# Performance work log

Measured on AMD Instinct MI355X. Metric: run time of the kernel, lower is better.

The kernel has to match this reference:

```python
import jax, jax.numpy as jnp
import numpy as np

B = 65536
EPS = 1e-5


def _cnot(psi, c, t):
    # psi: [B,2,2,2,2]; qubit q lives on axis q+1. CNOT flips target where control=1.
    c_ax, t_ax = c + 1, t + 1
    p0 = jax.lax.index_in_dim(psi, 0, c_ax, keepdims=True)
    p1 = jax.lax.index_in_dim(psi, 1, c_ax, keepdims=True)
    p1 = jnp.flip(p1, axis=t_ax)
    return jnp.concatenate([p0, p1], axis=c_ax)


def setup_inputs() -> dict:
    key = jax.random.key(0)
    x = jax.random.normal(key, (B, 1, 28, 28), dtype=jnp.float32)
    gamma = jnp.ones((4,), jnp.float32)   # BatchNorm1d(4) weight
    beta = jnp.zeros((4,), jnp.float32)   # BatchNorm1d(4) bias
    return {"x": x, "gamma": gamma, "beta": beta}


def reference(x, gamma, beta):
    bsz = x.shape[0]
    # avg_pool2d(x, 6): kernel=stride=6, no padding -> uses only the top-left 24x24
    pooled = x[:, :, :24, :24].reshape(bsz, 1, 4, 6, 4, 6).mean(axis=(3, 5))
    pooled = pooled.reshape(bsz, 16)
    theta = pooled[:, ::4]  # x[:, i*4] for i=0..3 -> [B,4] RY angles
    half = 0.5 * theta
    q = jnp.stack([jnp.cos(half), jnp.sin(half)], axis=-1)  # [B,4,2], RY|0> amplitudes (real)
    psi = jnp.einsum('bi,bj,bk,bl->bijkl', q[:, 0], q[:, 1], q[:, 2], q[:, 3])
    for c, t in ((0, 1), (1, 2), (2, 3), (3, 0)):
        psi = _cnot(psi, c, t)
    probs = psi * psi  # amplitudes are real
    signs = jnp.array([1.0, -1.0], jnp.float32)
    # <Z_i> = sum_s probs[s] * (-1)^{s_i}
    zs = [jnp.tensordot(probs, signs, axes=[[i + 1], [0]]).sum(axis=(1, 2, 3))
          for i in range(4)]
    out = jnp.stack(zs, axis=1)  # [B,4]
    # BatchNorm1d(4), training mode (biased batch variance)
    mean = out.mean(axis=0)
    var = out.var(axis=0)
    return gamma * (out - mean) / jnp.sqrt(var + EPS) + beta
```

## Files before the change

### kernel.cpp

```cpp
#include <hip/hip_runtime.h>

#define EPS 1e-5f


__global__ __launch_bounds__(256) void qnat_k1(const float* __restrict__ x,
                                               float* __restrict__ z_out,
                                               float* __restrict__ partials,
                                               int bsz) {
    const int t    = threadIdx.x;
    const int lane = t & 63;
    const int w    = t >> 6;
    const int imgBase = blockIdx.x * 16;

    float s1[4] = {0.f, 0.f, 0.f, 0.f};
    float s2[4] = {0.f, 0.f, 0.f, 0.f};

    #pragma unroll
    for (int iter = 0; iter < 4; ++iter) {
        const int img = imgBase + iter * 4 + w;
        float a0 = 0.f, a1 = 0.f, a2 = 0.f, a3 = 0.f;
        if (img < bsz) {
            const float* ip = x + (size_t)img * 784;
            #pragma unroll
            for (int r = 0; r < 3; ++r) {
                const int j = r * 64 + lane;
                const float4 v = *reinterpret_cast<const float4*>(ip + 4 * j);
                const int m = j % 7;
                const int p = j / 42;
                float contrib = 0.f;
                if (m == 0)      contrib = (v.x + v.y) + (v.z + v.w);
                else if (m == 1) contrib = v.x + v.y;
                a0 += (p == 0) ? contrib : 0.f;
                a1 += (p == 1) ? contrib : 0.f;
                a2 += (p == 2) ? contrib : 0.f;
                a3 += (p == 3) ? contrib : 0.f;
            }
        }
        #pragma unroll
        for (int off = 1; off < 64; off <<= 1) {
            a0 += __shfl_xor(a0, off, 64);
            a1 += __shfl_xor(a1, off, 64);
            a2 += __shfl_xor(a2, off, 64);
            a3 += __shfl_xor(a3, off, 64);
        }
        const float k = 1.0f / 36.0f;
        const float c0 = cosf(a0 * k), c1 = cosf(a1 * k);
        const float c2 = cosf(a2 * k), c3 = cosf(a3 * k);
        const float z1 = c0 * c1;
        const float z2 = z1 * c2;
        const float z3 = z2 * c3;
        const float z0 = c1 * c2 * c3;
        if (img < bsz) {
            if (lane == 0) {
                float4 zz; zz.x = z0; zz.y = z1; zz.z = z2; zz.w = z3;
                *reinterpret_cast<float4*>(z_out + (size_t)img * 4) = zz;
            }
            s1[0] += z0; s1[1] += z1; s1[2] += z2; s1[3] += z3;
            s2[0] += z0 * z0; s2[1] += z1 * z1; s2[2] += z2 * z2; s2[3] += z3 * z3;
        }
    }

    __shared__ float ps[4][8];
    if (lane == 0) {
        #pragma unroll
        for (int k = 0; k < 4; ++k) { ps[w][k] = s1[k]; ps[w][4 + k] = s2[k]; }
    }
    __syncthreads();
    if (t < 8) {
        partials[blockIdx.x * 8 + t] =
            (ps[0][t] + ps[1][t]) + (ps[2][t] + ps[3][t]);
    }
}

__global__ __launch_bounds__(1024) void qnat_stats(const float* __restrict__ partials,
                                                   const float* __restrict__ gamma,
                                                   float* __restrict__ stats,
                                                   int NB, int bsz) {
    const int t = threadIdx.x;
    float acc[8] = {0.f,0.f,0.f,0.f,0.f,0.f,0.f,0.f};
    for (int r = t; r < NB; r += 1024) {
        const float4 a = *reinterpret_cast<const float4*>(partials + r * 8);
        const float4 b = *reinterpret_cast<const float4*>(partials + r * 8 + 4);
        acc[0] += a.x; acc[1] += a.y; acc[2] += a.z; acc[3] += a.w;
        acc[4] += b.x; acc[5] += b.y; acc[6] += b.z; acc[7] += b.w;
    }
    #pragma unroll
    for (int off = 1; off < 64; off <<= 1)
        #pragma unroll
        for (int k = 0; k < 8; ++k) acc[k] += __shfl_xor(acc[k], off, 64);

    __shared__ float ls[16][8];
    const int wv = t >> 6, lane = t & 63;
    if (lane == 0)
        #pragma unroll
        for (int k = 0; k < 8; ++k) ls[wv][k] = acc[k];
    __syncthreads();
    if (t < 8) {
        float tot = 0.f;
        #pragma unroll
        for (int v = 0; v < 16; ++v) tot += ls[v][t];
        ls[0][t] = tot;
    }
    __syncthreads();
    if (t < 4) {
        const double invB = 1.0 / (double)bsz;
        const double m = (double)ls[0][t] * invB;
        const double var = (double)ls[0][4 + t] * invB - m * m;
        stats[t]     = (float)m;
        stats[4 + t] = gamma[t] * rsqrtf((float)var + EPS);
    }
}

__global__ __launch_bounds__(256) void qnat_k2(const float* __restrict__ z,
                                               const float* __restrict__ stats,
                                               const float* __restrict__ beta,
                                               float* __restrict__ out,
                                               int bsz) {
    const int t = blockIdx.x * blockDim.x + threadIdx.x;
    if (t < bsz) {
        const float4 zv = reinterpret_cast<const float4*>(z)[t];
        float4 o;
        o.x = (zv.x - stats[0]) * stats[4] + beta[0];
        o.y = (zv.y - stats[1]) * stats[5] + beta[1];
        o.z = (zv.z - stats[2]) * stats[6] + beta[2];
        o.w = (zv.w - stats[3]) * stats[7] + beta[3];
        reinterpret_cast<float4*>(out)[t] = o;
    }
}

extern "C" void kernel_launch(void* const* d_in, const int* in_sizes, int n_in,
                              void* d_out, int out_size, void* d_ws, size_t ws_size,
                              hipStream_t stream) {
    const float* x     = (const float*)d_in[0];
    const float* gamma = (const float*)d_in[1];
    const float* beta  = (const float*)d_in[2];
    float* out = (float*)d_out;

    const int bsz = in_sizes[0] / 784;
    const int NB  = (bsz + 15) / 16;

    float* stats    = (float*)d_ws;
    float* z        = (float*)((char*)d_ws + 4096);
    float* partials = (float*)((char*)d_ws + 4096 + (size_t)bsz * 16);

    qnat_k1   <<<NB, 256, 0, stream>>>(x, z, partials, bsz);
    qnat_stats<<<1, 1024, 0, stream>>>(partials, gamma, stats, NB, bsz);
    qnat_k2   <<<(bsz + 255) / 256, 256, 0, stream>>>(z, stats, beta, out, bsz);
}
```

Before: 45.74 us.

## Fuse pooling, batch stats and normalization into one cooperative grid-synced kernel

Replaces three launches (per-image kernel, single-block stats reduction, normalize pass) with one cooperative kernel of 1024 blocks. Each block keeps its z values in shared memory, writes per-block partial sums, waits at a grid-wide sync, then reduces all partials and normalizes its own images, so the z round trip through global memory and two launch gaps go away. It also skips the unused float4 loads in the last row group and swaps cosf for the faster, less accurate __cosf. The grid sync adds its own cost, and the hardcoded ipb cap of 64 means batches larger than 65536 would be silently truncated.

```diff
diff --git a/kernel.cpp b/kernel.cpp
--- a/kernel.cpp
+++ b/kernel.cpp
@@ -1,39 +1,53 @@
 #include <hip/hip_runtime.h>
+#include <hip/hip_cooperative_groups.h>
+
+namespace cg = cooperative_groups;
 
 #define EPS 1e-5f
+#define NBLK 1024
 
 
-__global__ __launch_bounds__(256) void qnat_k1(const float* __restrict__ x,
-                                               float* __restrict__ z_out,
-                                               float* __restrict__ partials,
-                                               int bsz) {
+__global__ __launch_bounds__(256, 4) void qnat_fused(const float* __restrict__ x,
+                                                     const float* __restrict__ gamma,
+                                                     const float* __restrict__ beta,
+                                                     float* __restrict__ out,
+                                                     float* __restrict__ partials,
+                                                     int bsz, int ipb) {
+    __shared__ float zsh[64][4];
+    __shared__ float ps[4][8];
+    __shared__ float red[4][8];
+    __shared__ float st[8];
+
     const int t    = threadIdx.x;
     const int lane = t & 63;
     const int w    = t >> 6;
-    const int imgBase = blockIdx.x * 16;
+    const int ipw  = ipb >> 2;
+    const int blk0 = blockIdx.x * ipb;
 
-    float s1[4] = {0.f, 0.f, 0.f, 0.f};
-    float s2[4] = {0.f, 0.f, 0.f, 0.f};
+    float s1[4] = {0.f,0.f,0.f,0.f};
+    float s2[4] = {0.f,0.f,0.f,0.f};
 
-    #pragma unroll
-    for (int iter = 0; iter < 4; ++iter) {
-        const int img = imgBase + iter * 4 + w;
+    for (int i = 0; i < ipw; ++i) {
+        const int il  = w * ipw + i;
+        const int img = blk0 + il;
         float a0 = 0.f, a1 = 0.f, a2 = 0.f, a3 = 0.f;
         if (img < bsz) {
             const float* ip = x + (size_t)img * 784;
             #pragma unroll
             for (int r = 0; r < 3; ++r) {
                 const int j = r * 64 + lane;
-                const float4 v = *reinterpret_cast<const float4*>(ip + 4 * j);
-                const int m = j % 7;
-                const int p = j / 42;
-                float contrib = 0.f;
-                if (m == 0)      contrib = (v.x + v.y) + (v.z + v.w);
-                else if (m == 1) contrib = v.x + v.y;
-                a0 += (p == 0) ? contrib : 0.f;
-                a1 += (p == 1) ? contrib : 0.f;
-                a2 += (p == 2) ? contrib : 0.f;
-                a3 += (p == 3) ? contrib : 0.f;
+                if (r < 2 || lane < 40) {
+                    const float4 v = *reinterpret_cast<const float4*>(ip + 4 * j);
+                    const int m = j % 7;
+                    const int p = j / 42;
+                    float contrib = 0.f;
+                    if (m == 0)      contrib = (v.x + v.y) + (v.z + v.w);
+                    else if (m == 1) contrib = v.x + v.y;
+                    a0 += (p == 0) ? contrib : 0.f;
+                    a1 += (p == 1) ? contrib : 0.f;
+                    a2 += (p == 2) ? contrib : 0.f;
+                    a3 += (p == 3) ? contrib : 0.f;
+                }
             }
         }
         #pragma unroll
@@ -44,8 +58,8 @@
             a3 += __shfl_xor(a3, off, 64);
         }
         const float k = 1.0f / 36.0f;
-        const float c0 = cosf(a0 * k), c1 = cosf(a1 * k);
-        const float c2 = cosf(a2 * k), c3 = cosf(a3 * k);
+        const float c0 = __cosf(a0 * k), c1 = __cosf(a1 * k);
+        const float c2 = __cosf(a2 * k), c3 = __cosf(a3 * k);
         const float z1 = c0 * c1;
         const float z2 = z1 * c2;
         const float z3 = z2 * c3;
@@ -53,78 +67,59 @@
         if (img < bsz) {
             if (lane == 0) {
                 float4 zz; zz.x = z0; zz.y = z1; zz.z = z2; zz.w = z3;
-                *reinterpret_cast<float4*>(z_out + (size_t)img * 4) = zz;
+                *reinterpret_cast<float4*>(&zsh[il][0]) = zz;
             }
             s1[0] += z0; s1[1] += z1; s1[2] += z2; s1[3] += z3;
-            s2[0] += z0 * z0; s2[1] += z1 * z1; s2[2] += z2 * z2; s2[3] += z3 * z3;
+            s2[0] += z0*z0; s2[1] += z1*z1; s2[2] += z2*z2; s2[3] += z3*z3;
         }
     }
-
-    __shared__ float ps[4][8];
     if (lane == 0) {
         #pragma unroll
-        for (int k = 0; k < 4; ++k) { ps[w][k] = s1[k]; ps[w][4 + k] = s2[k]; }
+        for (int k = 0; k < 4; ++k) { ps[w][k] = s1[k]; ps[w][4+k] = s2[k]; }
     }
     __syncthreads();
     if (t < 8) {
-        partials[blockIdx.x * 8 + t] =
-            (ps[0][t] + ps[1][t]) + (ps[2][t] + ps[3][t]);
+        partials[blockIdx.x * 8 + t] = (ps[0][t] + ps[1][t]) + (ps[2][t] + ps[3][t]);
     }
-}
 
-__global__ __launch_bounds__(1024) void qnat_stats(const float* __restrict__ partials,
-                                                   const float* __restrict__ gamma,
-                                                   float* __restrict__ stats,
-                                                   int NB, int bsz) {
-    const int t = threadIdx.x;
-    float acc[8] = {0.f,0.f,0.f,0.f,0.f,0.f,0.f,0.f};
-    for (int r = t; r < NB; r += 1024) {
-        const float4 a = *reinterpret_cast<const float4*>(partials + r * 8);
-        const float4 b = *reinterpret_cast<const float4*>(partials + r * 8 + 4);
-        acc[0] += a.x; acc[1] += a.y; acc[2] += a.z; acc[3] += a.w;
-        acc[4] += b.x; acc[5] += b.y; acc[6] += b.z; acc[7] += b.w;
+    cg::this_grid().sync();
+
+    {
+        const int k  = t & 7;
+        const int r0 = t >> 3;
+        float acc = 0.f;
+        #pragma unroll 4
+        for (int i = 0; i < NBLK / 32; ++i) {
+            acc += partials[(r0 + 32 * i) * 8 + k];
+        }
+        acc += __shfl_xor(acc, 8, 64);
+        acc += __shfl_xor(acc, 16, 64);
+        acc += __shfl_xor(acc, 32, 64);
+        if (lane < 8) red[w][lane] = acc;
+        __syncthreads();
+        if (t < 8) st[t] = (red[0][t] + red[1][t]) + (red[2][t] + red[3][t]);
+        __syncthreads();
+        if (t < 4) {
+            const double invB = 1.0 / (double)bsz;
+            const double m   = (double)st[t] * invB;
+            const double var = (double)st[4 + t] * invB - m * m;
+            st[t]     = (float)m;
+            st[4 + t] = gamma[t] * rsqrtf((float)var + EPS);
+        }
+        __syncthreads();
     }
-    #pragma unroll
-    for (int off = 1; off < 64; off <<= 1)
-        #pragma unroll
-        for (int k = 0; k < 8; ++k) acc[k] += __shfl_xor(acc[k], off, 64);
 
-    __shared__ float ls[16][8];
-    const int wv = t >> 6, lane = t & 63;
-    if (lane == 0)
-        #pragma unroll
-        for (int k = 0; k < 8; ++k) ls[wv][k] = acc[k];
-    __syncthreads();
-    if (t < 8) {
-        float tot = 0.f;
-        #pragma unroll
-        for (int v = 0; v < 16; ++v) tot += ls[v][t];
-        ls[0][t] = tot;
-    }
-    __syncthreads();
-    if (t < 4) {
-        const double invB = 1.0 / (double)bsz;
-        const double m = (double)ls[0][t] * invB;
-        const double var = (double)ls[0][4 + t] * invB - m * m;
-        stats[t]     = (float)m;
-        stats[4 + t] = gamma[t] * rsqrtf((float)var + EPS);
-    }
-}
-
-__global__ __launch_bounds__(256) void qnat_k2(const float* __restrict__ z,
-                                               const float* __restrict__ stats,
-                                               const float* __restrict__ beta,
-                                               float* __restrict__ out,
-                                               int bsz) {
-    const int t = blockIdx.x * blockDim.x + threadIdx.x;
-    if (t < bsz) {
-        const float4 zv = reinterpret_cast<const float4*>(z)[t];
-        float4 o;
-        o.x = (zv.x - stats[0]) * stats[4] + beta[0];
-        o.y = (zv.y - stats[1]) * stats[5] + beta[1];
-        o.z = (zv.z - stats[2]) * stats[6] + beta[2];
-        o.w = (zv.w - stats[3]) * stats[7] + beta[3];
-        reinterpret_cast<float4*>(out)[t] = o;
+    if (t < 64 && t < ipb) {
+        const int img = blk0 + t;
+        if (img < bsz) {
+            const float4 zv = *reinterpret_cast<const float4*>(&zsh[t][0]);
+            float4 o;
+            o.x = (zv.x - st[0]) * st[4] + beta[0];
+            o.y = (zv.y - st[1]) * st[5] + beta[1];
+            o.z = (zv.z - st[2]) * st[6] + beta[2];
+            o.w = (zv.w - st[3]) * st[7] + beta[3];
+            *reinterpret_cast<float4*>(out + (size_t)img * 4) = o;
+        }
     }
 }
 
@@ -137,13 +132,14 @@
     float* out = (float*)d_out;
 
     const int bsz = in_sizes[0] / 784;
-    const int NB  = (bsz + 15) / 16;
+    float* partials = (float*)d_ws;
 
-    float* stats    = (float*)d_ws;
-    float* z        = (float*)((char*)d_ws + 4096);
-    float* partials = (float*)((char*)d_ws + 4096 + (size_t)bsz * 16);
+    int ipb = (bsz + NBLK - 1) / NBLK;
+    ipb = (ipb + 3) & ~3;
+    if (ipb > 64) ipb = 64;
 
-    qnat_k1   <<<NB, 256, 0, stream>>>(x, z, partials, bsz);
-    qnat_stats<<<1, 1024, 0, stream>>>(partials, gamma, stats, NB, bsz);
-    qnat_k2   <<<(bsz + 255) / 256, 256, 0, stream>>>(z, stats, beta, out, bsz);
+    void* args[] = { (void*)&x, (void*)&gamma, (void*)&beta, (void*)&out,
+                     (void*)&partials, (void*)&bsz, (void*)&ipb };
+    hipLaunchCooperativeKernel((const void*)qnat_fused, dim3(NBLK), dim3(256),
+                               args, 0, stream);
 }
```

Result: slower. 162.8 us (+255.9%).

## Fuse batch-stat reduction into normalize kernel, skip unused loads, use fast cosine

Applied to the files above, without the earlier changes.

Drops the single-block stats kernel. Every block of the normalize kernel now redundantly reduces all per-block partials (4096 rows) itself, which saves one launch and one serialized step. The image loop also skips float4 loads past the 24 needed rows in its last pass, and cosf is replaced by the faster, lower-precision __cosf. The cost is that each of 256 blocks rereads 128KB of partials, and __cosf may lose accuracy.

```diff
diff --git a/kernel.cpp b/kernel.cpp
--- a/kernel.cpp
+++ b/kernel.cpp
@@ -24,16 +24,18 @@
             #pragma unroll
             for (int r = 0; r < 3; ++r) {
                 const int j = r * 64 + lane;
-                const float4 v = *reinterpret_cast<const float4*>(ip + 4 * j);
-                const int m = j % 7;
-                const int p = j / 42;
-                float contrib = 0.f;
-                if (m == 0)      contrib = (v.x + v.y) + (v.z + v.w);
-                else if (m == 1) contrib = v.x + v.y;
-                a0 += (p == 0) ? contrib : 0.f;
-                a1 += (p == 1) ? contrib : 0.f;
-                a2 += (p == 2) ? contrib : 0.f;
-                a3 += (p == 3) ? contrib : 0.f;
+                if (r < 2 || lane < 40) {
+                    const float4 v = *reinterpret_cast<const float4*>(ip + 4 * j);
+                    const int m = j % 7;
+                    const int p = j / 42;
+                    float contrib = 0.f;
+                    if (m == 0)      contrib = (v.x + v.y) + (v.z + v.w);
+                    else if (m == 1) contrib = v.x + v.y;
+                    a0 += (p == 0) ? contrib : 0.f;
+                    a1 += (p == 1) ? contrib : 0.f;
+                    a2 += (p == 2) ? contrib : 0.f;
+                    a3 += (p == 3) ? contrib : 0.f;
+                }
             }
         }
         #pragma unroll
@@ -44,8 +46,8 @@
             a3 += __shfl_xor(a3, off, 64);
         }
         const float k = 1.0f / 36.0f;
-        const float c0 = cosf(a0 * k), c1 = cosf(a1 * k);
-        const float c2 = cosf(a2 * k), c3 = cosf(a3 * k);
+        const float c0 = __cosf(a0 * k), c1 = __cosf(a1 * k);
+        const float c2 = __cosf(a2 * k), c3 = __cosf(a3 * k);
         const float z1 = c0 * c1;
         const float z2 = z1 * c2;
         const float z3 = z2 * c3;
@@ -67,64 +69,58 @@
     }
     __syncthreads();
     if (t < 8) {
-        partials[blockIdx.x * 8 + t] =
-            (ps[0][t] + ps[1][t]) + (ps[2][t] + ps[3][t]);
+        partials[blockIdx.x * 8 + t] = (ps[0][t] + ps[1][t]) + (ps[2][t] + ps[3][t]);
     }
 }
 
-__global__ __launch_bounds__(1024) void qnat_stats(const float* __restrict__ partials,
-                                                   const float* __restrict__ gamma,
-                                                   float* __restrict__ stats,
-                                                   int NB, int bsz) {
-    const int t = threadIdx.x;
+__global__ __launch_bounds__(256) void qnat_k2(const float* __restrict__ z,
+                                               const float* __restrict__ partials,
+                                               const float* __restrict__ gamma,
+                                               const float* __restrict__ beta,
+                                               float* __restrict__ out,
+                                               int NB, int bsz) {
+    __shared__ float red[4][8];
+    __shared__ float st[8];
+
+    const int t = threadIdx.x, lane = t & 63, w = t >> 6;
+
     float acc[8] = {0.f,0.f,0.f,0.f,0.f,0.f,0.f,0.f};
-    for (int r = t; r < NB; r += 1024) {
+    for (int r = t; r < NB; r += 256) {
         const float4 a = *reinterpret_cast<const float4*>(partials + r * 8);
         const float4 b = *reinterpret_cast<const float4*>(partials + r * 8 + 4);
         acc[0] += a.x; acc[1] += a.y; acc[2] += a.z; acc[3] += a.w;
         acc[4] += b.x; acc[5] += b.y; acc[6] += b.z; acc[7] += b.w;
     }
     #pragma unroll
-    for (int off = 1; off < 64; off <<= 1)
+    for (int off = 1; off < 64; off <<= 1) {
         #pragma unroll
         for (int k = 0; k < 8; ++k) acc[k] += __shfl_xor(acc[k], off, 64);
-
-    __shared__ float ls[16][8];
-    const int wv = t >> 6, lane = t & 63;
-    if (lane == 0)
+    }
+    if (lane == 0) {
         #pragma unroll
-        for (int k = 0; k < 8; ++k) ls[wv][k] = acc[k];
+        for (int k = 0; k < 8; ++k) red[w][k] = acc[k];
+    }
     __syncthreads();
-    if (t < 8) {
-        float tot = 0.f;
-        #pragma unroll
-        for (int v = 0; v < 16; ++v) tot += ls[v][t];
-        ls[0][t] = tot;
-    }
+    if (t < 8) st[t] = (red[0][t] + red[1][t]) + (red[2][t] + red[3][t]);
     __syncthreads();
     if (t < 4) {
         const double invB = 1.0 / (double)bsz;
-        const double m = (double)ls[0][t] * invB;
-        const double var = (double)ls[0][4 + t] * invB - m * m;
-        stats[t]     = (float)m;
-        stats[4 + t] = gamma[t] * rsqrtf((float)var + EPS);
+        const double m   = (double)st[t] * invB;
+        const double var = (double)st[4 + t] * invB - m * m;
+        st[t]     = (float)m;
+        st[4 + t] = gamma[t] * rsqrtf((float)var + EPS);
     }
-}
+    __syncthreads();
 
-__global__ __launch_bounds__(256) void qnat_k2(const float* __restrict__ z,
-                                               const float* __restrict__ stats,
-                                               const float* __restrict__ beta,
-                                               float* __restrict__ out,
-                                               int bsz) {
-    const int t = blockIdx.x * blockDim.x + threadIdx.x;
-    if (t < bsz) {
-        const float4 zv = reinterpret_cast<const float4*>(z)[t];
+    const int img = blockIdx.x * 256 + t;
+    if (img < bsz) {
+        const float4 zv = reinterpret_cast<const float4*>(z)[img];
         float4 o;
-        o.x = (zv.x - stats[0]) * stats[4] + beta[0];
-        o.y = (zv.y - stats[1]) * stats[5] + beta[1];
-        o.z = (zv.z - stats[2]) * stats[6] + beta[2];
-        o.w = (zv.w - stats[3]) * stats[7] + beta[3];
-        reinterpret_cast<float4*>(out)[t] = o;
+        o.x = (zv.x - st[0]) * st[4] + beta[0];
+        o.y = (zv.y - st[1]) * st[5] + beta[1];
+        o.z = (zv.z - st[2]) * st[6] + beta[2];
+        o.w = (zv.w - st[3]) * st[7] + beta[3];
+        reinterpret_cast<float4*>(out)[img] = o;
     }
 }
 
@@ -139,11 +135,9 @@
     const int bsz = in_sizes[0] / 784;
     const int NB  = (bsz + 15) / 16;
 
-    float* stats    = (float*)d_ws;
-    float* z        = (float*)((char*)d_ws + 4096);
-    float* partials = (float*)((char*)d_ws + 4096 + (size_t)bsz * 16);
+    float* z        = (float*)d_ws;
+    float* partials = (float*)((char*)d_ws + (size_t)bsz * 16);
 
-    qnat_k1   <<<NB, 256, 0, stream>>>(x, z, partials, bsz);
-    qnat_stats<<<1, 1024, 0, stream>>>(partials, gamma, stats, NB, bsz);
-    qnat_k2   <<<(bsz + 255) / 256, 256, 0, stream>>>(z, stats, beta, out, bsz);
+    qnat_k1<<<NB, 256, 0, stream>>>(x, z, partials, bsz);
+    qnat_k2<<<(bsz + 255) / 256, 256, 0, stream>>>(z, partials, gamma, beta, out, NB, bsz);
 }
```

Result: faster. 42.00 us (-8.2%).
